# Kernel tuning notes

Hardware: AMD Instinct MI355X
Metric: run time of the kernel (lower is better)

Reference implementation:

```python
import jax, jax.numpy as jnp
import numpy as np

B, T, D_IN = 128, 2048, 64
H, W_H, W_Y, D_OUT = 128, 256, 256, 64


def setup_inputs() -> dict:
    key = jax.random.key(0)
    ks = jax.random.split(key, 9)

    def lin(k, out_d, in_d):
        # approximate equinox Linear init scale (uniform-ish): 1/sqrt(fan_in)
        return jax.random.normal(k, (out_d, in_d), dtype=jnp.float32) / np.sqrt(in_d)

    return {
        "x": jax.random.normal(ks[0], (B, T, D_IN), dtype=jnp.float32),
        "hW1": lin(ks[1], W_H, H + D_IN),
        "hb1": jax.random.normal(ks[2], (W_H,), dtype=jnp.float32) * 0.01,
        "hW2": lin(ks[3], H, W_H),
        "hb2": jax.random.normal(ks[4], (H,), dtype=jnp.float32) * 0.01,
        "yW1": lin(ks[5], W_Y, H),
        "yb1": jax.random.normal(ks[6], (W_Y,), dtype=jnp.float32) * 0.01,
        "yW2": lin(ks[7], D_OUT, W_Y),
        "yb2": jax.random.normal(ks[8], (D_OUT,), dtype=jnp.float32) * 0.01,
    }


def reference(x, hW1, hb1, hW2, hb2, yW1, yb1, yW2, yb2):
    batch = x.shape[0]
    h0 = jnp.zeros((batch, H), dtype=x.dtype)

    def step(h, xt):  # h: [B,H], xt: [B,D_IN]
        hx = jnp.concatenate((h, xt), axis=1)               # [B, H+D_IN]
        h_new = jax.nn.silu(hx @ hW1.T + hb1) @ hW2.T + hb2  # hmlp: depth-2 MLP
        y = jax.nn.silu(h_new @ yW1.T + yb1) @ yW2.T + yb2   # ymlp: depth-2 MLP
        return h_new, y

    hidden, out = jax.lax.scan(step, h0, jnp.transpose(x, (1, 0, 2)))
    return jnp.transpose(out, (1, 0, 2)), hidden  # ([B,T,D_OUT], [B,H])
```

## Files before the change

### kernel.cpp

```cpp
#include <hip/hip_runtime.h>
#include <hip/hip_bf16.h>
#include <math.h>

#define B_   128
#define T_   2048
#define DIN  64
#define H_   128
#define WH_  256
#define WY_  256
#define DOUT 64

typedef __attribute__((ext_vector_type(8))) short short8;
typedef __attribute__((ext_vector_type(4))) float floatx4;

__device__ __forceinline__ void bar_lds() {
    asm volatile("s_waitcnt lgkmcnt(0)\n\ts_barrier" ::: "memory");
}

__device__ __forceinline__ short bf16_hi(float f) {
    __hip_bfloat16 h = __float2bfloat16(f);
    return *reinterpret_cast<short*>(&h);
}
__device__ __forceinline__ float bf16_val(short s) {
    __hip_bfloat16 h = *reinterpret_cast<__hip_bfloat16*>(&s);
    return __bfloat162float(h);
}

__device__ __forceinline__ float red_xor32(float v) {
    float d = v, s = v;
    asm volatile("v_permlane32_swap_b32 %0, %1" : "+v"(d), "+v"(s));
    return d + s;
}
__device__ __forceinline__ float red_xor16(float v) {
    float d = v, s = v;
    asm volatile("v_permlane16_swap_b32 %0, %1" : "+v"(d), "+v"(s));
    return d + s;
}

__global__ __launch_bounds__(512, 2) void rnn_phase1(
    const float* __restrict__ x,
    const float* __restrict__ hW1, const float* __restrict__ hb1,
    const float* __restrict__ hW2, const float* __restrict__ hb2,
    __hip_bfloat16* __restrict__ HallB,
    float* __restrict__ outF)
{
    const int b    = blockIdx.x;
    const int tid  = threadIdx.x;
    const int wave = tid >> 6, lane = tid & 63;

    __shared__ float hx[192];
    __shared__ float sl[256];

    const int f1 = wave * 32 + (lane & 31), kh = lane >> 5;
    const int f2 = wave * 16 + (lane & 15), kq = lane >> 4;

    float W1r[96];
#pragma unroll
    for (int jj = 0; jj < 24; ++jj)
        *(float4*)&W1r[jj * 4] = *(const float4*)&hW1[f1 * 192 + kh * 4 + jj * 8];
    float W2r[64];
#pragma unroll
    for (int jj = 0; jj < 16; ++jj)
        *(float4*)&W2r[jj * 4] = *(const float4*)&hW2[f2 * 256 + kq * 4 + jj * 16];

    const float b1v = hb1[f1];
    const float b2v = hb2[f2];

    if (tid < 128) hx[tid] = 0.f;
    float xreg = 0.f;
    if (tid >= 448) {
        const int l = tid - 448;
        const long xb = (long)b * (T_ * DIN);
        hx[128 + l] = x[xb + l];
        xreg        = x[xb + DIN + l];
    }
    __syncthreads();

    for (int t = 0; t < T_; ++t) {
        {
            float a0 = 0.f, a1 = 0.f, a2 = 0.f, a3 = 0.f;
            const float* hp = &hx[kh * 4];
#pragma unroll
            for (int jj = 0; jj < 24; ++jj) {
                const float4 h4 = *(const float4*)(hp + jj * 8);
                a0 += h4.x * W1r[jj * 4 + 0];
                a1 += h4.y * W1r[jj * 4 + 1];
                a2 += h4.z * W1r[jj * 4 + 2];
                a3 += h4.w * W1r[jj * 4 + 3];
            }
            float v = red_xor32((a0 + a1) + (a2 + a3));
            v += b1v;
            const float s = v / (1.f + expf(-v));
            if (lane < 32) sl[f1] = s;
        }
        bar_lds();

        {
            float c0 = 0.f, c1 = 0.f, c2 = 0.f, c3 = 0.f;
            const float* sp = &sl[kq * 4];
#pragma unroll
            for (int jj = 0; jj < 16; ++jj) {
                const float4 s4 = *(const float4*)(sp + jj * 16);
                c0 += s4.x * W2r[jj * 4 + 0];
                c1 += s4.y * W2r[jj * 4 + 1];
                c2 += s4.z * W2r[jj * 4 + 2];
                c3 += s4.w * W2r[jj * 4 + 3];
            }
            float hv = red_xor16((c0 + c1) + (c2 + c3));
            hv = red_xor32(hv);
            hv += b2v;
            if (lane < 16) {
                hx[f2] = hv;
                HallB[((long)t * B_ + b) * H_ + f2] = __float2bfloat16(hv);
            }
            if (tid >= 448) {
                const int l = tid - 448;
                hx[128 + l] = xreg;
                const int tn = (t + 2 < T_) ? (t + 2) : (T_ - 1);
                xreg = x[(long)b * (T_ * DIN) + (long)tn * DIN + l];
            }
        }
        bar_lds();
    }

    if (tid < 128)
        outF[(long)B_ * T_ * DOUT + (long)b * H_ + tid] = hx[tid];
}

__global__ __launch_bounds__(256) void presplit(
    const float* __restrict__ yW1, const float* __restrict__ yW2,
    short* __restrict__ Y1f, short* __restrict__ Y2f)
{
    const int i = blockIdx.x * 256 + threadIdx.x;
    if (i < 32768) {
        const int j = i & 7, lane = (i >> 3) & 63, ks = (i >> 9) & 3, nt = i >> 11;
        const float v = yW1[(nt * 16 + (lane & 15)) * 128 + (lane >> 4) * 8 + ks * 32 + j];
        const short h = bf16_hi(v);
        Y1f[i]         = h;
        Y1f[32768 + i] = bf16_hi(v - bf16_val(h));
    }
    if (i < 16384) {
        const int j = i & 7, lane = (i >> 3) & 63, ks = (i >> 9) & 7, nt2 = i >> 12;
        const float v = yW2[(nt2 * 16 + (lane & 15)) * 256 + (lane >> 4) * 8 + ks * 32 + j];
        const short h = bf16_hi(v);
        Y2f[i]         = h;
        Y2f[16384 + i] = bf16_hi(v - bf16_val(h));
    }
}

__global__ __launch_bounds__(256) void rnn_phase2(
    const __hip_bfloat16* __restrict__ HallB,
    const float* __restrict__ yb1, const float* __restrict__ yb2,
    const short* __restrict__ Y1f, const short* __restrict__ Y2f,
    float* __restrict__ out)
{
    __shared__ short u_lds[4][2][16 * 256];

    const int tid  = threadIdx.x;
    const int wave = tid >> 6, lane = tid & 63;
    const int l15  = lane & 15, lg = lane >> 4;
    const long pair = (long)blockIdx.x * 4 + wave;
    const long r0   = pair * 32;
    const floatx4 zero4 = {0.f, 0.f, 0.f, 0.f};
    const short* Hs = (const short*)HallB;

    short8 aH[2][4];
#pragma unroll
    for (int p = 0; p < 2; ++p)
#pragma unroll
        for (int ks = 0; ks < 4; ++ks)
            aH[p][ks] = *(const short8*)(Hs + (r0 + p * 16 + l15) * 128 + lg * 8 + ks * 32);

#pragma unroll
    for (int nt = 0; nt < 16; ++nt) {
        floatx4 accA = zero4, accB = zero4;
#pragma unroll
        for (int ks = 0; ks < 4; ++ks) {
            const short8 bhi = *(const short8*)(Y1f + ((nt * 4 + ks) * 512 + lane * 8));
            const short8 blo = *(const short8*)(Y1f + 32768 + ((nt * 4 + ks) * 512 + lane * 8));
            accA = __builtin_amdgcn_mfma_f32_16x16x32_bf16(aH[0][ks], bhi, accA, 0, 0, 0);
            accA = __builtin_amdgcn_mfma_f32_16x16x32_bf16(aH[0][ks], blo, accA, 0, 0, 0);
            accB = __builtin_amdgcn_mfma_f32_16x16x32_bf16(aH[1][ks], bhi, accB, 0, 0, 0);
            accB = __builtin_amdgcn_mfma_f32_16x16x32_bf16(aH[1][ks], blo, accB, 0, 0, 0);
        }
        const int col  = nt * 16 + l15;
        const float bias = yb1[col];
#pragma unroll
        for (int r = 0; r < 4; ++r) {
            const int row = lg * 4 + r;
            int byte = row * 512 + col * 2;
            byte ^= ((row & 7) << 4);
            float v = accA[r] + bias;
            *(short*)((char*)u_lds[wave][0] + byte) = bf16_hi(v / (1.f + __expf(-v)));
            v = accB[r] + bias;
            *(short*)((char*)u_lds[wave][1] + byte) = bf16_hi(v / (1.f + __expf(-v)));
        }
    }
    asm volatile("s_waitcnt lgkmcnt(0)" ::: "memory");

    floatx4 acc2A[4] = {zero4, zero4, zero4, zero4};
    floatx4 acc2B[4] = {zero4, zero4, zero4, zero4};
#pragma unroll
    for (int ks = 0; ks < 8; ++ks) {
        int byte = l15 * 512 + (lg * 8 + ks * 32) * 2;
        byte ^= ((l15 & 7) << 4);
        const short8 aUa = *(const short8*)((char*)u_lds[wave][0] + byte);
        const short8 aUb = *(const short8*)((char*)u_lds[wave][1] + byte);
#pragma unroll
        for (int nt = 0; nt < 4; ++nt) {
            const short8 bhi = *(const short8*)(Y2f + ((nt * 8 + ks) * 512 + lane * 8));
            const short8 blo = *(const short8*)(Y2f + 16384 + ((nt * 8 + ks) * 512 + lane * 8));
            acc2A[nt] = __builtin_amdgcn_mfma_f32_16x16x32_bf16(aUa, bhi, acc2A[nt], 0, 0, 0);
            acc2A[nt] = __builtin_amdgcn_mfma_f32_16x16x32_bf16(aUa, blo, acc2A[nt], 0, 0, 0);
            acc2B[nt] = __builtin_amdgcn_mfma_f32_16x16x32_bf16(aUb, bhi, acc2B[nt], 0, 0, 0);
            acc2B[nt] = __builtin_amdgcn_mfma_f32_16x16x32_bf16(aUb, blo, acc2B[nt], 0, 0, 0);
        }
    }

#pragma unroll
    for (int nt = 0; nt < 4; ++nt) {
        const int col  = nt * 16 + l15;
        const float bias = yb2[col];
#pragma unroll
        for (int r = 0; r < 4; ++r) {
            {
                const long R  = r0 + lg * 4 + r;
                const long bb = R & (B_ - 1);
                const long tt = R >> 7;
                out[bb * (T_ * DOUT) + tt * DOUT + col] = acc2A[nt][r] + bias;
            }
            {
                const long R  = r0 + 16 + lg * 4 + r;
                const long bb = R & (B_ - 1);
                const long tt = R >> 7;
                out[bb * (T_ * DOUT) + tt * DOUT + col] = acc2B[nt][r] + bias;
            }
        }
    }
}

extern "C" void kernel_launch(void* const* d_in, const int* in_sizes, int n_in,
                              void* d_out, int out_size, void* d_ws, size_t ws_size,
                              hipStream_t stream) {
    const float* x   = (const float*)d_in[0];
    const float* hW1 = (const float*)d_in[1];
    const float* hb1 = (const float*)d_in[2];
    const float* hW2 = (const float*)d_in[3];
    const float* hb2 = (const float*)d_in[4];
    const float* yW1 = (const float*)d_in[5];
    const float* yb1 = (const float*)d_in[6];
    const float* yW2 = (const float*)d_in[7];
    const float* yb2 = (const float*)d_in[8];

    float* out = (float*)d_out;
    __hip_bfloat16* HallB = (__hip_bfloat16*)d_ws;
    const size_t hallBytes = (size_t)T_ * B_ * H_ * sizeof(__hip_bfloat16);
    short* Y1f = (short*)((char*)d_ws + hallBytes);
    short* Y2f = Y1f + 65536;

    rnn_phase1<<<128, 512, 0, stream>>>(x, hW1, hb1, hW2, hb2, HallB, out);
    presplit<<<128, 256, 0, stream>>>(yW1, yW2, Y1f, Y2f);
    rnn_phase2<<<2048, 256, 0, stream>>>(HallB, yb1, yb2, Y1f, Y2f, out);
}
```

Baseline: 2.210 ms.

## Register-block 4 hidden features per lane to reuse LDS loads in recurrent MLP

```diff
diff --git a/kernel.cpp b/kernel.cpp
--- a/kernel.cpp
+++ b/kernel.cpp
@@ -35,6 +35,11 @@
     float d = v, s = v;
     asm volatile("v_permlane16_swap_b32 %0, %1" : "+v"(d), "+v"(s));
     return d + s;
+}
+__device__ __forceinline__ float red_xor8(float v) {
+    const int s = __builtin_amdgcn_update_dpp(
+        0, __float_as_int(v), 0x128 , 0xF, 0xF, true);
+    return v + __int_as_float(s);
 }
 
 __global__ __launch_bounds__(512, 2) void rnn_phase1(
@@ -51,20 +56,28 @@
     __shared__ float hx[192];
     __shared__ float sl[256];
 
-    const int f1 = wave * 32 + (lane & 31), kh = lane >> 5;
-    const int f2 = wave * 16 + (lane & 15), kq = lane >> 4;
-
-    float W1r[96];
-#pragma unroll
-    for (int jj = 0; jj < 24; ++jj)
-        *(float4*)&W1r[jj * 4] = *(const float4*)&hW1[f1 * 192 + kh * 4 + jj * 8];
-    float W2r[64];
-#pragma unroll
-    for (int jj = 0; jj < 16; ++jj)
-        *(float4*)&W2r[jj * 4] = *(const float4*)&hW2[f2 * 256 + kq * 4 + jj * 16];
-
-    const float b1v = hb1[f1];
-    const float b2v = hb2[f2];
+    const int kq  = lane >> 3;
+    const int fo  = wave * 8 + (lane & 7);
+    const int fb1 = fo * 4;
+    const int fb2 = fo * 2;
+
+    float W1r[4][24];
+#pragma unroll
+    for (int f = 0; f < 4; ++f)
+#pragma unroll
+        for (int jj = 0; jj < 6; ++jj)
+            *(float4*)&W1r[f][jj * 4] =
+                *(const float4*)&hW1[(fb1 + f) * 192 + kq * 4 + jj * 32];
+    float W2r[2][32];
+#pragma unroll
+    for (int f = 0; f < 2; ++f)
+#pragma unroll
+        for (int jj = 0; jj < 8; ++jj)
+            *(float4*)&W2r[f][jj * 4] =
+                *(const float4*)&hW2[(fb2 + f) * 256 + kq * 4 + jj * 32];
+
+    const float4 b1v = *(const float4*)&hb1[fb1];
+    const float2 b2v = *(const float2*)&hb2[fb2];
 
     if (tid < 128) hx[tid] = 0.f;
     float xreg = 0.f;
@@ -79,39 +92,50 @@
     for (int t = 0; t < T_; ++t) {
         {
             float a0 = 0.f, a1 = 0.f, a2 = 0.f, a3 = 0.f;
-            const float* hp = &hx[kh * 4];
-#pragma unroll
-            for (int jj = 0; jj < 24; ++jj) {
-                const float4 h4 = *(const float4*)(hp + jj * 8);
-                a0 += h4.x * W1r[jj * 4 + 0];
-                a1 += h4.y * W1r[jj * 4 + 1];
-                a2 += h4.z * W1r[jj * 4 + 2];
-                a3 += h4.w * W1r[jj * 4 + 3];
-            }
-            float v = red_xor32((a0 + a1) + (a2 + a3));
-            v += b1v;
-            const float s = v / (1.f + expf(-v));
-            if (lane < 32) sl[f1] = s;
+            const float* hp = &hx[kq * 4];
+#pragma unroll
+            for (int jj = 0; jj < 6; ++jj) {
+                const float4 h4 = *(const float4*)(hp + jj * 32);
+                a0 += h4.x * W1r[0][jj*4+0] + h4.y * W1r[0][jj*4+1]
+                    + h4.z * W1r[0][jj*4+2] + h4.w * W1r[0][jj*4+3];
+                a1 += h4.x * W1r[1][jj*4+0] + h4.y * W1r[1][jj*4+1]
+                    + h4.z * W1r[1][jj*4+2] + h4.w * W1r[1][jj*4+3];
+                a2 += h4.x * W1r[2][jj*4+0] + h4.y * W1r[2][jj*4+1]
+                    + h4.z * W1r[2][jj*4+2] + h4.w * W1r[2][jj*4+3];
+                a3 += h4.x * W1r[3][jj*4+0] + h4.y * W1r[3][jj*4+1]
+                    + h4.z * W1r[3][jj*4+2] + h4.w * W1r[3][jj*4+3];
+            }
+            float v0 = red_xor32(red_xor16(red_xor8(a0))) + b1v.x;
+            float v1 = red_xor32(red_xor16(red_xor8(a1))) + b1v.y;
+            float v2 = red_xor32(red_xor16(red_xor8(a2))) + b1v.z;
+            float v3 = red_xor32(red_xor16(red_xor8(a3))) + b1v.w;
+            const float s0 = v0 / (1.f + expf(-v0));
+            const float s1 = v1 / (1.f + expf(-v1));
+            const float s2 = v2 / (1.f + expf(-v2));
+            const float s3 = v3 / (1.f + expf(-v3));
+            if (lane < 8) *(float4*)&sl[fb1] = make_float4(s0, s1, s2, s3);
         }
         bar_lds();
 
         {
-            float c0 = 0.f, c1 = 0.f, c2 = 0.f, c3 = 0.f;
+            float c0 = 0.f, c1 = 0.f;
             const float* sp = &sl[kq * 4];
 #pragma unroll
-            for (int jj = 0; jj < 16; ++jj) {
-                const float4 s4 = *(const float4*)(sp + jj * 16);
-                c0 += s4.x * W2r[jj * 4 + 0];
-                c1 += s4.y * W2r[jj * 4 + 1];
-                c2 += s4.z * W2r[jj * 4 + 2];
-                c3 += s4.w * W2r[jj * 4 + 3];
-            }
-            float hv = red_xor16((c0 + c1) + (c2 + c3));
-            hv = red_xor32(hv);
-            hv += b2v;
-            if (lane < 16) {
-                hx[f2] = hv;
-                HallB[((long)t * B_ + b) * H_ + f2] = __float2bfloat16(hv);
+            for (int jj = 0; jj < 8; ++jj) {
+                const float4 s4 = *(const float4*)(sp + jj * 32);
+                c0 += s4.x * W2r[0][jj*4+0] + s4.y * W2r[0][jj*4+1]
+                    + s4.z * W2r[0][jj*4+2] + s4.w * W2r[0][jj*4+3];
+                c1 += s4.x * W2r[1][jj*4+0] + s4.y * W2r[1][jj*4+1]
+                    + s4.z * W2r[1][jj*4+2] + s4.w * W2r[1][jj*4+3];
+            }
+            const float h0 = red_xor32(red_xor16(red_xor8(c0))) + b2v.x;
+            const float h1 = red_xor32(red_xor16(red_xor8(c1))) + b2v.y;
+            if (lane < 8) {
+                *(float2*)&hx[fb2] = make_float2(h0, h1);
+                const unsigned pk =
+                    (unsigned)(unsigned short)bf16_hi(h0) |
+                    ((unsigned)(unsigned short)bf16_hi(h1) << 16);
+                ((unsigned*)HallB)[((long)t * B_ + b) * (H_ / 2) + fo] = pk;
             }
             if (tid >= 448) {
                 const int l = tid - 448;
```

Result: slower. 2.988 ms (+35.2%).
